# Kernel optimization log

Measured on AMD Instinct MI355X. Metric: run time of the kernel, lower is better.

Reference implementation:

```python
import jax, jax.numpy as jnp
import numpy as np

VOCAB, D = 32000, 128
B, R, C, T = 8, 100, 64, 32


def setup_inputs() -> dict:
    key = jax.random.key(0)
    k1, k2, k3 = jax.random.split(key, 3)
    x = jax.random.randint(k1, (B, R, C, T), 0, VOCAB, dtype=jnp.int32)
    W_embed = jax.random.normal(k2, (VOCAB, D), dtype=jnp.float32)
    w_pred = jax.random.normal(k3, (1, D), dtype=jnp.float32) * (1.0 / np.sqrt(D))
    b_pred = jnp.zeros((1,), dtype=jnp.float32)
    return {"x": x, "W_embed": W_embed, "w_pred": w_pred, "b_pred": b_pred}


def reference(x, W_embed, w_pred, b_pred):
    # Embedding gather for every cell token at once: [B,R,C,T,D]
    emb = W_embed[x]
    # Mean over tokens within each cell: [B,R,C,D]
    pooled = emb.mean(axis=-2)
    # Dropout is identity in eval mode. Exact (erf) GELU as in torch nn.GELU default.
    act = jax.nn.gelu(pooled, approximate=False)
    # Linear(D -> 1), squeeze to scalar per cell: [B,R,C]
    out = jnp.einsum('brcd,d->brc', act, w_pred[0]) + b_pred[0]
    return out
```

## Files before the change

kernel.cpp:

```cpp
#include <hip/hip_runtime.h>
#include <hip/hip_bf16.h>
#include <math.h>
#include <string.h>

constexpr int VOCAB  = 32000;
constexpr int D      = 128;
constexpr int T      = 32;
constexpr int NCELLS = 8 * 100 * 64;
constexpr int NCHUNK = 2;
constexpr int CDIM   = D / NCHUNK;

constexpr float QSCALE = 30.0f;
constexpr float QINV   = 1.0f / (QSCALE * (float)T);

typedef int v16i __attribute__((ext_vector_type(16)));

__device__ inline float gelu_fast(float xv) {
    const float is2 = 0.70710678118654752440f;
    float y  = xv * is2;
    float av = fabsf(y);
    float t  = __builtin_amdgcn_rcpf(__builtin_fmaf(0.3275911f, av, 1.0f));
    float p  = 0.254829592f + t * (-0.284496736f + t * (1.421413741f
             + t * (-1.453152027f + t * 1.061405429f)));
    float e  = __expf(-av * av);
    float er = 1.0f - p * t * e;
    er = copysignf(er, y);
    return 0.5f * xv * (1.0f + er);
}

__device__ inline unsigned char q8(float w) {
    int q = __float2int_rn(w * QSCALE);
    q = q < -127 ? -127 : (q > 127 ? 127 : q);
    return (unsigned char)(q + 128);
}

__global__ __launch_bounds__(256) void convert_W_kernel(
    const float* __restrict__ W, unsigned char* __restrict__ Wq,
    float* __restrict__ out)
{
    const int i = blockIdx.x * blockDim.x + threadIdx.x;
    const int v = i >> 5;
    const int k = i & 31;
    const int chunk = k >> 4;
    const int sub   = k & 15;

    float4 src = reinterpret_cast<const float4*>(W)[i];
    uchar4 o;
    o.x = q8(src.x); o.y = q8(src.y); o.z = q8(src.z); o.w = q8(src.w);
    reinterpret_cast<uchar4*>(Wq)[(size_t)chunk * (VOCAB * 16) + (size_t)v * 16 + sub] = o;

    if (i < NCELLS) out[i] = 0.0f;
}

__global__ __launch_bounds__(256) void gather_kernel(
    const int*           __restrict__ x,
    const unsigned char* __restrict__ Wq,
    const float*         __restrict__ w_pred,
    const float*         __restrict__ b_pred,
    float*               __restrict__ out)
{
    const int lane = threadIdx.x & 63;

    const int slot  = blockIdx.x & 7;
    const int chunk = slot >> 2;
    const int sub   = slot & 3;
    const int g     = blockIdx.x >> 3;
    const int cell  = __builtin_amdgcn_readfirstlane(
        ((g << 2) + sub) * 4 + (threadIdx.x >> 6));

    const int* __restrict__ xc = x + (size_t)cell * T;

    v16i ia, ib;
    asm volatile("s_load_dwordx16 %0, %2, 0x0\n\t"
                 "s_load_dwordx16 %1, %2, 0x40\n\t"
                 "s_waitcnt lgkmcnt(0)"
                 : "=&s"(ia), "=&s"(ib)
                 : "s"(xc));

    const unsigned char* __restrict__ tb = Wq + (size_t)chunk * (VOCAB * CDIM);

    uint32_t rv[32];
    #pragma unroll
    for (int t = 0; t < 16; ++t) {
        rv[t]      = tb[(size_t)ia[t] * CDIM + lane];
        rv[t + 16] = tb[(size_t)ib[t] * CDIM + lane];
    }

    uint32_t a0 = 0, a1 = 0, a2 = 0, a3 = 0;
    #pragma unroll
    for (int t = 0; t < 32; t += 4) {
        a0 += rv[t];
        a1 += rv[t + 1];
        a2 += rv[t + 2];
        a3 += rv[t + 3];
    }
    uint32_t total = (a0 + a1) + (a2 + a3);

    float p  = (float)((int)total - 128 * T) * QINV;
    float gl = gelu_fast(p);
    float wv = w_pred[chunk * CDIM + lane];
    float s  = gl * wv;

    #pragma unroll
    for (int off = 32; off >= 1; off >>= 1)
        s += __shfl_xor(s, off, 64);

    if (lane == 0) {
        if (chunk == 0) s += b_pred[0];
        atomicAdd(&out[cell], s);
    }
}

extern "C" void kernel_launch(void* const* d_in, const int* in_sizes, int n_in,
                              void* d_out, int out_size, void* d_ws, size_t ws_size,
                              hipStream_t stream) {
    const int*   x      = (const int*)  d_in[0];
    const float* W      = (const float*)d_in[1];
    const float* w_pred = (const float*)d_in[2];
    const float* b_pred = (const float*)d_in[3];
    float*       out    = (float*)d_out;
    unsigned char* Wq   = (unsigned char*)d_ws;

    const int conv_groups = VOCAB * D / 4;
    convert_W_kernel<<<conv_groups / 256, 256, 0, stream>>>(W, Wq, out);

    gather_kernel<<<NCHUNK * (NCELLS / 4), 256, 0, stream>>>(x, Wq, w_pred, b_pred, out);
}
```

Before: 105.6 us.

## Gather two int8 dims per lane via ushort loads, drop chunk split and atomics

The quantized table is now stored in natural row-major order, and each lane loads a 16-bit pair covering two embedding dims. The two bytes are accumulated together in one 32-bit add and split afterwards into low and high sums. This halves the number of blocks, removes the two-chunk split, and replaces the atomicAdd (and the zeroing of out) with a direct store. It trades one wider load per token for two byte loads in separate blocks, so the load instruction count and the launch of half the blocks go away. The cost is a little extra ALU per lane (a second GELU and masking).

```diff
diff --git a/kernel.cpp b/kernel.cpp
--- a/kernel.cpp
+++ b/kernel.cpp
@@ -7,8 +7,6 @@
 constexpr int D      = 128;
 constexpr int T      = 32;
 constexpr int NCELLS = 8 * 100 * 64;
-constexpr int NCHUNK = 2;
-constexpr int CDIM   = D / NCHUNK;
 
 constexpr float QSCALE = 30.0f;
 constexpr float QINV   = 1.0f / (QSCALE * (float)T);
@@ -35,21 +33,13 @@
 }
 
 __global__ __launch_bounds__(256) void convert_W_kernel(
-    const float* __restrict__ W, unsigned char* __restrict__ Wq,
-    float* __restrict__ out)
+    const float* __restrict__ W, unsigned char* __restrict__ Wq)
 {
     const int i = blockIdx.x * blockDim.x + threadIdx.x;
-    const int v = i >> 5;
-    const int k = i & 31;
-    const int chunk = k >> 4;
-    const int sub   = k & 15;
-
     float4 src = reinterpret_cast<const float4*>(W)[i];
     uchar4 o;
     o.x = q8(src.x); o.y = q8(src.y); o.z = q8(src.z); o.w = q8(src.w);
-    reinterpret_cast<uchar4*>(Wq)[(size_t)chunk * (VOCAB * 16) + (size_t)v * 16 + sub] = o;
-
-    if (i < NCELLS) out[i] = 0.0f;
+    reinterpret_cast<uchar4*>(Wq)[i] = o;
 }
 
 __global__ __launch_bounds__(256) void gather_kernel(
@@ -60,13 +50,8 @@
     float*               __restrict__ out)
 {
     const int lane = threadIdx.x & 63;
-
-    const int slot  = blockIdx.x & 7;
-    const int chunk = slot >> 2;
-    const int sub   = slot & 3;
-    const int g     = blockIdx.x >> 3;
-    const int cell  = __builtin_amdgcn_readfirstlane(
-        ((g << 2) + sub) * 4 + (threadIdx.x >> 6));
+    const int cell = __builtin_amdgcn_readfirstlane(
+        blockIdx.x * 4 + (threadIdx.x >> 6));
 
     const int* __restrict__ xc = x + (size_t)cell * T;
 
@@ -77,38 +62,41 @@
                  : "=&s"(ia), "=&s"(ib)
                  : "s"(xc));
 
-    const unsigned char* __restrict__ tb = Wq + (size_t)chunk * (VOCAB * CDIM);
+    const ushort* __restrict__ tb = reinterpret_cast<const ushort*>(Wq);
 
     uint32_t rv[32];
     #pragma unroll
     for (int t = 0; t < 16; ++t) {
-        rv[t]      = tb[(size_t)ia[t] * CDIM + lane];
-        rv[t + 16] = tb[(size_t)ib[t] * CDIM + lane];
+        rv[t]      = tb[(size_t)ia[t] * 64 + lane];
+        rv[t + 16] = tb[(size_t)ib[t] * 64 + lane];
     }
 
-    uint32_t a0 = 0, a1 = 0, a2 = 0, a3 = 0;
+    uint32_t sA = 0, sB = 0, lA = 0, lB = 0;
     #pragma unroll
-    for (int t = 0; t < 32; t += 4) {
-        a0 += rv[t];
-        a1 += rv[t + 1];
-        a2 += rv[t + 2];
-        a3 += rv[t + 3];
+    for (int t = 0; t < 32; t += 2) {
+        sA += rv[t];
+        lA += rv[t] & 0xFFu;
+        sB += rv[t + 1];
+        lB += rv[t + 1] & 0xFFu;
     }
-    uint32_t total = (a0 + a1) + (a2 + a3);
+    uint32_t S = sA + sB;
+    uint32_t L = lA + lB;
+    uint32_t H = (S - L) >> 8;
 
-    float p  = (float)((int)total - 128 * T) * QINV;
-    float gl = gelu_fast(p);
-    float wv = w_pred[chunk * CDIM + lane];
-    float s  = gl * wv;
+    float p0 = (float)((int)L - 128 * T) * QINV;
+    float p1 = (float)((int)H - 128 * T) * QINV;
+    float g0 = gelu_fast(p0);
+    float g1 = gelu_fast(p1);
+
+    float2 wv = reinterpret_cast<const float2*>(w_pred)[lane];
+    float s = __builtin_fmaf(g0, wv.x, g1 * wv.y);
 
     #pragma unroll
     for (int off = 32; off >= 1; off >>= 1)
         s += __shfl_xor(s, off, 64);
 
-    if (lane == 0) {
-        if (chunk == 0) s += b_pred[0];
-        atomicAdd(&out[cell], s);
-    }
+    if (lane == 0)
+        out[cell] = s + b_pred[0];
 }
 
 extern "C" void kernel_launch(void* const* d_in, const int* in_sizes, int n_in,
@@ -122,7 +110,7 @@
     unsigned char* Wq   = (unsigned char*)d_ws;
 
     const int conv_groups = VOCAB * D / 4;
-    convert_W_kernel<<<conv_groups / 256, 256, 0, stream>>>(W, Wq, out);
+    convert_W_kernel<<<conv_groups / 256, 256, 0, stream>>>(W, Wq);
 
-    gather_kernel<<<NCHUNK * (NCELLS / 4), 256, 0, stream>>>(x, Wq, w_pred, b_pred, out);
+    gather_kernel<<<NCELLS / 4, 256, 0, stream>>>(x, Wq, w_pred, b_pred, out);
 }
```

Measured after the change: 91.87 us, median of 2. -13.0%, faster.
